# Kernel optimization log

Hardware: AMD Instinct MI355X
Metric: run time of the kernel (lower is better)

The kernel has to match this reference:

```python
import jax, jax.numpy as jnp
import numpy as np

B, T, N, M, D = 4, 2, 2048, 2048, 3

def _pairwise_sq(a, b):
    # a: [B,N,D], b: [B,M,D] -> squared euclidean distances [B,N,M]
    a2 = jnp.sum(a * a, axis=-1)
    b2 = jnp.sum(b * b, axis=-1)
    ab = jnp.einsum('bnd,bmd->bnm', a, b)
    return jnp.maximum(a2[:, :, None] + b2[:, None, :] - 2.0 * ab, 0.0)


def setup_inputs() -> dict:
    key = jax.random.key(0)
    k1, k2, k3, k4 = jax.random.split(key, 4)
    x = jax.random.uniform(k1, (B, T, N, D), dtype=jnp.float32)
    # m_hat is the frozen motion model's output; small motions keep chamfer mask active
    m_hat = jax.random.uniform(k2, (B, 1, N, D), dtype=jnp.float32) * 0.02
    y_hat0 = jax.random.uniform(k3, (B, 1, M, D), dtype=jnp.float32)
    y_hat1 = jax.random.uniform(k4, (B, 1, M, D), dtype=jnp.float32)
    return {'x': x, 'm_hat': m_hat, 'y_hat0': y_hat0, 'y_hat1': y_hat1}


def reference(x, m_hat, y_hat0, y_hat1):
    sg = jax.lax.stop_gradient
    x_t0 = x[:, 0, :, :3]              # [B,N,3]
    x_t1 = x[:, 1, :, :3]              # [B,N,3]
    x_t1_hat = x_t0 + m_hat[:, 0]      # [B,N,3]

    # chamfer(x_t1_hat, x_t1): squared NN distances both ways
    d = _pairwise_sq(x_t1_hat, x_t1)   # [B,N,N]
    dist1 = jnp.min(d, axis=-1)
    dist2 = jnp.min(d, axis=-2)
    loss_chamfer = dist1.mean(axis=-1) + dist2.mean(axis=-1)          # [B]
    mask_chamfer = sg((loss_chamfer < 0.1).astype(x.dtype))[:, None, None, None]

    y0 = y_hat0[:, 0]                  # [B,M,3]
    dists = jnp.sqrt(_pairwise_sq(y0, x_t0))                          # [B,M,N]
    x_cat = jnp.concatenate([x_t0, x_t1], axis=1)                     # [B,2N,3]
    dists2 = jnp.sqrt(_pairwise_sq(y0, x_cat))                        # [B,M,2N]

    min_dists = jnp.min(dists, axis=-1)        # [B,M]
    min_indices = jnp.argmin(dists, axis=-1)   # [B,M]
    min_dists2 = jnp.min(dists2, axis=-1)      # [B,M]

    mask_dist = sg((min_dists < 0.05).astype(x.dtype))[:, None, :, None]      # [B,1,M,1]
    mask_dist_neg = sg((min_dists2 > 0.2).astype(x.dtype))[:, None, :, None]  # [B,1,M,1]

    nearest_m = jnp.take_along_axis(m_hat[:, 0], min_indices[:, :, None], axis=1)  # [B,M,3]

    # chamfer(x_t0, y_hat0): only dist1 used, masked mean over entries < 0.1
    c1 = jnp.min(_pairwise_sq(x_t0, y0), axis=-1)                     # [B,N]
    sel = c1 < 0.1
    loss_dist = jnp.sum(jnp.where(sel, c1, 0.0)) / jnp.maximum(jnp.sum(sel.astype(c1.dtype)), 1.0)

    pred = (y_hat1 - y_hat0) * mask_chamfer * mask_dist               # [B,1,M,3]
    tgt = nearest_m[:, None, :, :] * mask_chamfer * mask_dist
    loss_dynamic = jnp.mean((pred - tgt) ** 2)

    my_hat_static = (y_hat1 - y_hat0) * mask_dist_neg
    loss_static = jnp.mean(my_hat_static ** 2)

    return (loss_dynamic, loss_static, loss_dist)
```

## Files before the change

kernel.cpp:

```cpp
#include <hip/hip_runtime.h>
#include <math.h>

#define BATCH 4
#define NPTS  2048
#define NT    256
#define ROWS_PT 4
#define CPB     64
#define COLCHUNKS (NPTS / CPB)
#define ROWHALVES 2
#define ROWS_TOT  (BATCH * NPTS)
#define RB_BLOCKS (ROWS_TOT / 128)

#define OFF_PD1   0
#define OFF_PD2   (COLCHUNKS * ROWS_TOT)
#define OFF_PC1   (2 * COLCHUNKS * ROWS_TOT)
#define OFF_PRM3  (3 * COLCHUNKS * ROWS_TOT)
#define OFF_PRM2  (4 * COLCHUNKS * ROWS_TOT)
#define OFF_BLK   (6 * COLCHUNKS * ROWS_TOT)
#define INF_BITS 0x7f800000u

typedef unsigned long long ull;

__device__ __forceinline__ float sqnorm3(float x, float y, float z) {
    return __fadd_rn(__fadd_rn(__fmul_rn(x, x), __fmul_rn(y, y)), __fmul_rn(z, z));
}

#define SRC_T0  0
#define SRC_T1  1
#define SRC_T1H 2
#define SRC_Y0  3

__device__ __forceinline__ float4 make_point(int src, bool col, int b, int i,
    const float* __restrict__ x, const float* __restrict__ m_hat,
    const float* __restrict__ y_hat0)
{
    float px, py, pz;
    if (src == SRC_Y0) {
        const float* p = y_hat0 + ((size_t)b * NPTS + i) * 3;
        px = p[0]; py = p[1]; pz = p[2];
    } else if (src == SRC_T1) {
        const float* p = x + ((size_t)(b * 2 + 1) * NPTS + i) * 3;
        px = p[0]; py = p[1]; pz = p[2];
    } else {
        const float* p = x + ((size_t)(b * 2 + 0) * NPTS + i) * 3;
        px = p[0]; py = p[1]; pz = p[2];
        if (src == SRC_T1H) {
            const float* mh = m_hat + ((size_t)b * NPTS + i) * 3;
            px += mh[0]; py += mh[1]; pz += mh[2];
        }
    }
    float w = sqnorm3(px, py, pz);
    if (col) { px *= -2.0f; py *= -2.0f; pz *= -2.0f; }
    return make_float4(px, py, pz, w);
}

__device__ __forceinline__ ull shfl_xor_u64(ull v, int m) {
    int lo = __shfl_xor((int)(v & 0xFFFFFFFFull), m);
    int hi = __shfl_xor((int)(v >> 32), m);
    return ((ull)(unsigned)hi << 32) | (unsigned)lo;
}

__device__ __forceinline__ float dist_sq_raw(const float4& a, const float4& q) {
    float s = a.x * q.x + a.y * q.y + a.z * q.z;
    float u = __fadd_rn(a.w, q.w);
    return __fadd_rn(u, s);
}

__global__ __launch_bounds__(NT) void pairwise_kernel(
    const float* __restrict__ x, const float* __restrict__ m_hat,
    const float* __restrict__ y_hat0, float* __restrict__ ws)
{
    __shared__ float4 tile[CPB];

    int tid = threadIdx.x;
    int rowHalf  = blockIdx.x >> 5;
    int colChunk = blockIdx.x & 31;
    int b    = blockIdx.y;
    int prob = blockIdx.z;

    int rsrc, csrc, outOff;
    switch (prob) {
        case 0:  rsrc = SRC_T1H; csrc = SRC_T1;  outOff = OFF_PD1;  break;
        case 1:  rsrc = SRC_T1;  csrc = SRC_T1H; outOff = OFF_PD2;  break;
        case 2:  rsrc = SRC_Y0;  csrc = SRC_T0;  outOff = -1;       break;
        case 3:  rsrc = SRC_Y0;  csrc = SRC_T1;  outOff = OFF_PRM3; break;
        default: rsrc = SRC_T0;  csrc = SRC_Y0;  outOff = OFF_PC1;  break;
    }

    int colBase = colChunk * CPB;
    if (tid < CPB) tile[tid] = make_point(csrc, true, b, colBase + tid, x, m_hat, y_hat0);

    int r0 = rowHalf * (NT * ROWS_PT) + tid;
    float4 a[ROWS_PT];
    #pragma unroll
    for (int k = 0; k < ROWS_PT; ++k)
        a[k] = make_point(rsrc, false, b, r0 + k * NT, x, m_hat, y_hat0);

    __syncthreads();

    if (prob == 2) {
        float best[ROWS_PT];
        int bestIdx[ROWS_PT];
        #pragma unroll
        for (int k = 0; k < ROWS_PT; ++k) { best[k] = __uint_as_float(INF_BITS); bestIdx[k] = 0; }
        for (int c = 0; c < CPB; ++c) {
            float4 q = tile[c];
            #pragma unroll
            for (int k = 0; k < ROWS_PT; ++k) {
                float d = fmaxf(dist_sq_raw(a[k], q), 0.0f);
                if (d < best[k]) { best[k] = d; bestIdx[k] = c; }
            }
        }
        ull* prm2 = (ull*)(ws + OFF_PRM2);
        #pragma unroll
        for (int k = 0; k < ROWS_PT; ++k) {
            ull key = ((ull)__float_as_uint(best[k]) << 32) |
                      (unsigned)(colBase + bestIdx[k]);
            prm2[(size_t)colChunk * ROWS_TOT + b * NPTS + r0 + k * NT] = key;
        }
    } else {
        float best[ROWS_PT];
        #pragma unroll
        for (int k = 0; k < ROWS_PT; ++k) best[k] = __uint_as_float(INF_BITS);
        for (int c = 0; c < CPB; ++c) {
            float4 q = tile[c];
            #pragma unroll
            for (int k = 0; k < ROWS_PT; ++k)
                best[k] = fminf(best[k], dist_sq_raw(a[k], q));
        }
        #pragma unroll
        for (int k = 0; k < ROWS_PT; ++k)
            ws[outOff + (size_t)colChunk * ROWS_TOT + b * NPTS + r0 + k * NT] = best[k];
    }
}

__global__ __launch_bounds__(NT) void rowreduce_kernel(
    const float* __restrict__ m_hat, const float* __restrict__ y_hat0,
    const float* __restrict__ y_hat1, float* __restrict__ ws)
{
    int tid  = threadIdx.x;
    int row  = blockIdx.x * 128 + (tid >> 1);
    int half = tid & 1;
    int b    = row >> 11;

    const ull* prm2 = (const ull*)(ws + OFF_PRM2);

    float d1m = __uint_as_float(INF_BITS), d2m = d1m, c1m = d1m, r3m = d1m;
    ull k2 = ~0ull;
    #pragma unroll
    for (int c = 0; c < 16; ++c) {
        int idx = (half * 16 + c) * ROWS_TOT + row;
        d1m = fminf(d1m, ws[OFF_PD1 + idx]);
        d2m = fminf(d2m, ws[OFF_PD2 + idx]);
        c1m = fminf(c1m, ws[OFF_PC1 + idx]);
        r3m = fminf(r3m, ws[OFF_PRM3 + idx]);
        ull kk = prm2[idx];
        k2 = (kk < k2) ? kk : k2;
    }
    d1m = fminf(d1m, __shfl_xor(d1m, 1));
    d2m = fminf(d2m, __shfl_xor(d2m, 1));
    c1m = fminf(c1m, __shfl_xor(c1m, 1));
    r3m = fminf(r3m, __shfl_xor(r3m, 1));
    { ull o = shfl_xor_u64(k2, 1); k2 = (o < k2) ? o : k2; }

    d1m = fmaxf(d1m, 0.0f);
    d2m = fmaxf(d2m, 0.0f);
    c1m = fmaxf(c1m, 0.0f);
    r3m = fmaxf(r3m, 0.0f);

    float d2sq = __uint_as_float((unsigned)(k2 >> 32));
    unsigned idxm = (unsigned)(k2 & 0xFFFFFFFFull);
    float md   = (sqrtf(d2sq) < 0.05f) ? 1.0f : 0.0f;
    float dcat = fminf(d2sq, r3m);
    float mneg = (sqrtf(dcat) > 0.2f) ? 1.0f : 0.0f;

    const float* p0 = y_hat0 + (size_t)row * 3;
    const float* p1 = y_hat1 + (size_t)row * 3;
    const float* nm = m_hat + ((size_t)b * NPTS + idxm) * 3;

    float dyn = 0.f, stat = 0.f;
    #pragma unroll
    for (int k = 0; k < 3; ++k) {
        float diff = p1[k] - p0[k];
        float e = md * (diff - nm[k]);
        dyn += e * e;
        float s = mneg * diff;
        stat += s * s;
    }
    float cs = (c1m < 0.1f) ? c1m : 0.f;
    float cn = (c1m < 0.1f) ? 1.f  : 0.f;
    float s1 = d1m, s2 = d2m;
    if (half) { s1 = s2 = cs = cn = dyn = stat = 0.f; }

    #pragma unroll
    for (int off = 32; off > 0; off >>= 1) {
        s1  += __shfl_down(s1,  off);
        s2  += __shfl_down(s2,  off);
        cs  += __shfl_down(cs,  off);
        cn  += __shfl_down(cn,  off);
        dyn += __shfl_down(dyn, off);
        stat+= __shfl_down(stat,off);
    }
    __shared__ float sm[4][6];
    int wv = tid >> 6, ln = tid & 63;
    if (ln == 0) {
        sm[wv][0] = s1; sm[wv][1] = s2; sm[wv][2] = cs;
        sm[wv][3] = cn; sm[wv][4] = dyn; sm[wv][5] = stat;
    }
    __syncthreads();
    if (tid == 0) {
        #pragma unroll
        for (int j = 0; j < 6; ++j)
            ws[OFF_BLK + blockIdx.x * 8 + j] = sm[0][j] + sm[1][j] + sm[2][j] + sm[3][j];
    }
}

__global__ void final_kernel(const float* __restrict__ ws, float* __restrict__ out)
{
    int lane = threadIdx.x;
    float v[6];
    #pragma unroll
    for (int j = 0; j < 6; ++j) v[j] = ws[OFF_BLK + lane * 8 + j];
    #pragma unroll
    for (int off = 8; off > 0; off >>= 1) {
        #pragma unroll
        for (int j = 0; j < 6; ++j) {
            float t = __shfl_down(v[j], off);
            if (((lane & 15) + off) < 16) v[j] += t;
        }
    }
    __shared__ float bs[4][6];
    if ((lane & 15) == 0) {
        #pragma unroll
        for (int j = 0; j < 6; ++j) bs[lane >> 4][j] = v[j];
    }
    __syncthreads();
    if (lane == 0) {
        float dyn = 0.f, stat = 0.f, cs = 0.f, cn = 0.f;
        for (int b = 0; b < 4; ++b) {
            float lc = bs[b][0] / (float)NPTS + bs[b][1] / (float)NPTS;
            float maskc = (lc < 0.1f) ? 1.0f : 0.0f;
            dyn  += maskc * bs[b][4];
            stat += bs[b][5];
            cs   += bs[b][2];
            cn   += bs[b][3];
        }
        const float denom = (float)(BATCH * NPTS * 3);
        out[0] = dyn / denom;
        out[1] = stat / denom;
        out[2] = cs / fmaxf(cn, 1.0f);
    }
}

extern "C" void kernel_launch(void* const* d_in, const int* in_sizes, int n_in,
                              void* d_out, int out_size, void* d_ws, size_t ws_size,
                              hipStream_t stream)
{
    const float* x      = (const float*)d_in[0];
    const float* m_hat  = (const float*)d_in[1];
    const float* y_hat0 = (const float*)d_in[2];
    const float* y_hat1 = (const float*)d_in[3];
    float* ws  = (float*)d_ws;
    float* out = (float*)d_out;

    pairwise_kernel<<<dim3(ROWHALVES * COLCHUNKS, BATCH, 5), dim3(NT), 0, stream>>>(
        x, m_hat, y_hat0, ws);
    rowreduce_kernel<<<dim3(RB_BLOCKS), dim3(NT), 0, stream>>>(
        m_hat, y_hat0, y_hat1, ws);
    final_kernel<<<dim3(1), dim3(64), 0, stream>>>(ws, out);
}
```

Baseline: 84.67 us.

## Share distance tiles for row and column mins, register-tile 8x8, fuse final reduce

Each distance matrix is now computed once, and both its row minima and column minima are reduced from the same 128x128 tile. This cuts the pairwise work from five matrix passes to three. Each thread now computes an 8x8 register tile from padded shared-memory row and column tiles, using shuffle and shared reductions for the partial minima. The separate final kernel is removed: the last rowreduce block, found through an atomic counter, does the global reduction. In exchange, the new counter needs a reset inside the pairwise kernel and some column partials are computed in swapped operand order, so rounding may differ slightly.

```diff
diff --git a/kernel.cpp b/kernel.cpp
--- a/kernel.cpp
+++ b/kernel.cpp
@@ -4,20 +4,23 @@
 #define BATCH 4
 #define NPTS  2048
 #define NT    256
-#define ROWS_PT 4
-#define CPB     64
-#define COLCHUNKS (NPTS / CPB)
-#define ROWHALVES 2
-#define ROWS_TOT  (BATCH * NPTS)
+#define TM    128
+#define TN    128
+#define CH    (NPTS / TN)
+#define ROWS_TOT (BATCH * NPTS)
 #define RB_BLOCKS (ROWS_TOT / 128)
-
-#define OFF_PD1   0
-#define OFF_PD2   (COLCHUNKS * ROWS_TOT)
-#define OFF_PC1   (2 * COLCHUNKS * ROWS_TOT)
-#define OFF_PRM3  (3 * COLCHUNKS * ROWS_TOT)
-#define OFF_PRM2  (4 * COLCHUNKS * ROWS_TOT)
-#define OFF_BLK   (6 * COLCHUNKS * ROWS_TOT)
+#define CHUNK_F (CH * ROWS_TOT)
+
+#define OFF_AROW 0
+#define OFF_ACOL (1 * CHUNK_F)
+#define OFF_BCOL (2 * CHUNK_F)
+#define OFF_CROW (3 * CHUNK_F)
+#define OFF_BKEY (4 * CHUNK_F)
+#define OFF_BLK  (6 * CHUNK_F)
+#define OFF_CTR  (OFF_BLK + RB_BLOCKS * 8)
 #define INF_BITS 0x7f800000u
+
+#define PIDX(i) ((i) + ((i) >> 3))
 
 typedef unsigned long long ull;
 
@@ -70,91 +73,187 @@
     const float* __restrict__ x, const float* __restrict__ m_hat,
     const float* __restrict__ y_hat0, float* __restrict__ ws)
 {
-    __shared__ float4 tile[CPB];
+    __shared__ float4 rowT[TM + TM / 8];
+    __shared__ float4 colT[TN + TN / 8];
+    __shared__ float  colRed[4][TN];
 
     int tid = threadIdx.x;
-    int rowHalf  = blockIdx.x >> 5;
-    int colChunk = blockIdx.x & 31;
-    int b    = blockIdx.y;
-    int prob = blockIdx.z;
-
-    int rsrc, csrc, outOff;
-    switch (prob) {
-        case 0:  rsrc = SRC_T1H; csrc = SRC_T1;  outOff = OFF_PD1;  break;
-        case 1:  rsrc = SRC_T1;  csrc = SRC_T1H; outOff = OFF_PD2;  break;
-        case 2:  rsrc = SRC_Y0;  csrc = SRC_T0;  outOff = -1;       break;
-        case 3:  rsrc = SRC_Y0;  csrc = SRC_T1;  outOff = OFF_PRM3; break;
-        default: rsrc = SRC_T0;  csrc = SRC_Y0;  outOff = OFF_PC1;  break;
-    }
-
-    int colBase = colChunk * CPB;
-    if (tid < CPB) tile[tid] = make_point(csrc, true, b, colBase + tid, x, m_hat, y_hat0);
-
-    int r0 = rowHalf * (NT * ROWS_PT) + tid;
-    float4 a[ROWS_PT];
-    #pragma unroll
-    for (int k = 0; k < ROWS_PT; ++k)
-        a[k] = make_point(rsrc, false, b, r0 + k * NT, x, m_hat, y_hat0);
-
+    int rowChunk = blockIdx.x >> 4;
+    int colChunk = blockIdx.x & 15;
+    int b   = blockIdx.y;
+    int mat = blockIdx.z;
+
+    if (blockIdx.x == 0 && b == 0 && mat == 0 && tid == 0)
+        ((unsigned*)ws)[OFF_CTR] = 0u;
+
+    int rsrc, csrc;
+    if (mat == 0)      { rsrc = SRC_T1H; csrc = SRC_T1; }
+    else if (mat == 1) { rsrc = SRC_Y0;  csrc = SRC_T0; }
+    else               { rsrc = SRC_Y0;  csrc = SRC_T1; }
+
+    int rowBase = rowChunk * TM;
+    int colBase = colChunk * TN;
+
+    if (tid < TM) {
+        rowT[PIDX(tid)] = make_point(rsrc, false, b, rowBase + tid, x, m_hat, y_hat0);
+    } else {
+        int t = tid - TM;
+        colT[PIDX(t)] = make_point(csrc, true, b, colBase + t, x, m_hat, y_hat0);
+    }
     __syncthreads();
 
-    if (prob == 2) {
-        float best[ROWS_PT];
-        int bestIdx[ROWS_PT];
-        #pragma unroll
-        for (int k = 0; k < ROWS_PT; ++k) { best[k] = __uint_as_float(INF_BITS); bestIdx[k] = 0; }
-        for (int c = 0; c < CPB; ++c) {
-            float4 q = tile[c];
-            #pragma unroll
-            for (int k = 0; k < ROWS_PT; ++k) {
-                float d = fmaxf(dist_sq_raw(a[k], q), 0.0f);
-                if (d < best[k]) { best[k] = d; bestIdx[k] = c; }
-            }
-        }
-        ull* prm2 = (ull*)(ws + OFF_PRM2);
-        #pragma unroll
-        for (int k = 0; k < ROWS_PT; ++k) {
-            ull key = ((ull)__float_as_uint(best[k]) << 32) |
-                      (unsigned)(colBase + bestIdx[k]);
-            prm2[(size_t)colChunk * ROWS_TOT + b * NPTS + r0 + k * NT] = key;
+    int tx = tid & 15, ty = tid >> 4;
+    float4 a[8], q[8];
+    #pragma unroll
+    for (int i = 0; i < 8; ++i) a[i] = rowT[PIDX(ty * 8 + i)];
+    #pragma unroll
+    for (int j = 0; j < 8; ++j) q[j] = colT[PIDX(tx * 8 + j)];
+
+    if (mat == 1) {
+        float rbest[8], cmin[8];
+        int ridx[8];
+        #pragma unroll
+        for (int i = 0; i < 8; ++i) {
+            rbest[i] = __uint_as_float(INF_BITS);
+            cmin[i]  = __uint_as_float(INF_BITS);
+            ridx[i]  = 0;
+        }
+        #pragma unroll
+        for (int j = 0; j < 8; ++j) {
+            #pragma unroll
+            for (int i = 0; i < 8; ++i) {
+                float d = dist_sq_raw(a[i], q[j]);
+                cmin[j] = fminf(cmin[j], d);
+                float dc = fmaxf(d, 0.0f);
+                if (dc < rbest[i]) { rbest[i] = dc; ridx[i] = j; }
+            }
+        }
+        ull key[8];
+        #pragma unroll
+        for (int i = 0; i < 8; ++i)
+            key[i] = ((ull)__float_as_uint(rbest[i]) << 32) |
+                     (unsigned)(colBase + tx * 8 + ridx[i]);
+        #pragma unroll
+        for (int m = 1; m < 16; m <<= 1) {
+            #pragma unroll
+            for (int i = 0; i < 8; ++i) {
+                ull o = shfl_xor_u64(key[i], m);
+                key[i] = (o < key[i]) ? o : key[i];
+            }
+        }
+        if (tx == 0) {
+            ull* o = (ull*)(ws + OFF_BKEY) +
+                     (size_t)colChunk * ROWS_TOT + b * NPTS + rowBase + ty * 8;
+            #pragma unroll
+            for (int i = 0; i < 8; ++i) o[i] = key[i];
+        }
+        #pragma unroll
+        for (int j = 0; j < 8; ++j) {
+            cmin[j] = fminf(cmin[j], __shfl_xor(cmin[j], 16));
+            cmin[j] = fminf(cmin[j], __shfl_xor(cmin[j], 32));
+        }
+        int w = tid >> 6;
+        if ((tid & 63) < 16) {
+            #pragma unroll
+            for (int j = 0; j < 8; ++j) colRed[w][tx * 8 + j] = cmin[j];
+        }
+        __syncthreads();
+        if (tid < TN) {
+            float v = fminf(fminf(colRed[0][tid], colRed[1][tid]),
+                            fminf(colRed[2][tid], colRed[3][tid]));
+            ws[OFF_BCOL + (size_t)rowChunk * ROWS_TOT + b * NPTS + colBase + tid] = v;
+        }
+    } else if (mat == 0) {
+        float rmin[8], cmin[8];
+        #pragma unroll
+        for (int i = 0; i < 8; ++i) {
+            rmin[i] = __uint_as_float(INF_BITS);
+            cmin[i] = __uint_as_float(INF_BITS);
+        }
+        #pragma unroll
+        for (int j = 0; j < 8; ++j) {
+            #pragma unroll
+            for (int i = 0; i < 8; ++i) {
+                float d = dist_sq_raw(a[i], q[j]);
+                rmin[i] = fminf(rmin[i], d);
+                cmin[j] = fminf(cmin[j], d);
+            }
+        }
+        #pragma unroll
+        for (int m = 1; m < 16; m <<= 1) {
+            #pragma unroll
+            for (int i = 0; i < 8; ++i)
+                rmin[i] = fminf(rmin[i], __shfl_xor(rmin[i], m));
+        }
+        if (tx == 0) {
+            float* o = ws + OFF_AROW +
+                       (size_t)colChunk * ROWS_TOT + b * NPTS + rowBase + ty * 8;
+            *(float4*)(o)     = make_float4(rmin[0], rmin[1], rmin[2], rmin[3]);
+            *(float4*)(o + 4) = make_float4(rmin[4], rmin[5], rmin[6], rmin[7]);
+        }
+        #pragma unroll
+        for (int j = 0; j < 8; ++j) {
+            cmin[j] = fminf(cmin[j], __shfl_xor(cmin[j], 16));
+            cmin[j] = fminf(cmin[j], __shfl_xor(cmin[j], 32));
+        }
+        int w = tid >> 6;
+        if ((tid & 63) < 16) {
+            #pragma unroll
+            for (int j = 0; j < 8; ++j) colRed[w][tx * 8 + j] = cmin[j];
+        }
+        __syncthreads();
+        if (tid < TN) {
+            float v = fminf(fminf(colRed[0][tid], colRed[1][tid]),
+                            fminf(colRed[2][tid], colRed[3][tid]));
+            ws[OFF_ACOL + (size_t)rowChunk * ROWS_TOT + b * NPTS + colBase + tid] = v;
         }
     } else {
-        float best[ROWS_PT];
-        #pragma unroll
-        for (int k = 0; k < ROWS_PT; ++k) best[k] = __uint_as_float(INF_BITS);
-        for (int c = 0; c < CPB; ++c) {
-            float4 q = tile[c];
-            #pragma unroll
-            for (int k = 0; k < ROWS_PT; ++k)
-                best[k] = fminf(best[k], dist_sq_raw(a[k], q));
-        }
-        #pragma unroll
-        for (int k = 0; k < ROWS_PT; ++k)
-            ws[outOff + (size_t)colChunk * ROWS_TOT + b * NPTS + r0 + k * NT] = best[k];
+        float rmin[8];
+        #pragma unroll
+        for (int i = 0; i < 8; ++i) rmin[i] = __uint_as_float(INF_BITS);
+        #pragma unroll
+        for (int j = 0; j < 8; ++j) {
+            #pragma unroll
+            for (int i = 0; i < 8; ++i)
+                rmin[i] = fminf(rmin[i], dist_sq_raw(a[i], q[j]));
+        }
+        #pragma unroll
+        for (int m = 1; m < 16; m <<= 1) {
+            #pragma unroll
+            for (int i = 0; i < 8; ++i)
+                rmin[i] = fminf(rmin[i], __shfl_xor(rmin[i], m));
+        }
+        if (tx == 0) {
+            float* o = ws + OFF_CROW +
+                       (size_t)colChunk * ROWS_TOT + b * NPTS + rowBase + ty * 8;
+            *(float4*)(o)     = make_float4(rmin[0], rmin[1], rmin[2], rmin[3]);
+            *(float4*)(o + 4) = make_float4(rmin[4], rmin[5], rmin[6], rmin[7]);
+        }
     }
 }
 
 __global__ __launch_bounds__(NT) void rowreduce_kernel(
     const float* __restrict__ m_hat, const float* __restrict__ y_hat0,
-    const float* __restrict__ y_hat1, float* __restrict__ ws)
+    const float* __restrict__ y_hat1, float* __restrict__ ws,
+    float* __restrict__ out)
 {
     int tid  = threadIdx.x;
     int row  = blockIdx.x * 128 + (tid >> 1);
     int half = tid & 1;
     int b    = row >> 11;
 
-    const ull* prm2 = (const ull*)(ws + OFF_PRM2);
+    const ull* bkey = (const ull*)(ws + OFF_BKEY);
 
     float d1m = __uint_as_float(INF_BITS), d2m = d1m, c1m = d1m, r3m = d1m;
     ull k2 = ~0ull;
     #pragma unroll
-    for (int c = 0; c < 16; ++c) {
-        int idx = (half * 16 + c) * ROWS_TOT + row;
-        d1m = fminf(d1m, ws[OFF_PD1 + idx]);
-        d2m = fminf(d2m, ws[OFF_PD2 + idx]);
-        c1m = fminf(c1m, ws[OFF_PC1 + idx]);
-        r3m = fminf(r3m, ws[OFF_PRM3 + idx]);
-        ull kk = prm2[idx];
+    for (int c = 0; c < 8; ++c) {
+        int idx = (half * 8 + c) * ROWS_TOT + row;
+        d1m = fminf(d1m, ws[OFF_AROW + idx]);
+        d2m = fminf(d2m, ws[OFF_ACOL + idx]);
+        c1m = fminf(c1m, ws[OFF_BCOL + idx]);
+        r3m = fminf(r3m, ws[OFF_CROW + idx]);
+        ull kk = bkey[idx];
         k2 = (kk < k2) ? kk : k2;
     }
     d1m = fminf(d1m, __shfl_xor(d1m, 1));
@@ -202,6 +301,7 @@
         stat+= __shfl_down(stat,off);
     }
     __shared__ float sm[4][6];
+    __shared__ int lastBlock;
     int wv = tid >> 6, ln = tid & 63;
     if (ln == 0) {
         sm[wv][0] = s1; sm[wv][1] = s2; sm[wv][2] = cs;
@@ -210,45 +310,62 @@
     __syncthreads();
     if (tid == 0) {
         #pragma unroll
+        for (int j = 0; j < 6; ++j) {
+            float v = sm[0][j] + sm[1][j] + sm[2][j] + sm[3][j];
+            __hip_atomic_store(ws + OFF_BLK + blockIdx.x * 8 + j, v,
+                               __ATOMIC_RELAXED, __HIP_MEMORY_SCOPE_AGENT);
+        }
+        __threadfence();
+        unsigned old = atomicAdd(((unsigned*)ws) + OFF_CTR, 1u);
+        lastBlock = (old == RB_BLOCKS - 1) ? 1 : 0;
+    }
+    __syncthreads();
+
+    if (lastBlock != 0 && tid < 64) {
+        __threadfence();
+        int lane = tid;
+        float v[6];
+        #pragma unroll
         for (int j = 0; j < 6; ++j)
-            ws[OFF_BLK + blockIdx.x * 8 + j] = sm[0][j] + sm[1][j] + sm[2][j] + sm[3][j];
-    }
-}
-
-__global__ void final_kernel(const float* __restrict__ ws, float* __restrict__ out)
-{
-    int lane = threadIdx.x;
-    float v[6];
-    #pragma unroll
-    for (int j = 0; j < 6; ++j) v[j] = ws[OFF_BLK + lane * 8 + j];
-    #pragma unroll
-    for (int off = 8; off > 0; off >>= 1) {
+            v[j] = __hip_atomic_load(ws + OFF_BLK + lane * 8 + j,
+                                     __ATOMIC_RELAXED, __HIP_MEMORY_SCOPE_AGENT);
+        #pragma unroll
+        for (int off = 8; off > 0; off >>= 1) {
+            #pragma unroll
+            for (int j = 0; j < 6; ++j) {
+                float t = __shfl_down(v[j], off);
+                if (((lane & 15) + off) < 16) v[j] += t;
+            }
+        }
+        float g1[6], g2[6], g3[6];
         #pragma unroll
         for (int j = 0; j < 6; ++j) {
-            float t = __shfl_down(v[j], off);
-            if (((lane & 15) + off) < 16) v[j] += t;
-        }
-    }
-    __shared__ float bs[4][6];
-    if ((lane & 15) == 0) {
-        #pragma unroll
-        for (int j = 0; j < 6; ++j) bs[lane >> 4][j] = v[j];
-    }
-    __syncthreads();
-    if (lane == 0) {
-        float dyn = 0.f, stat = 0.f, cs = 0.f, cn = 0.f;
-        for (int b = 0; b < 4; ++b) {
-            float lc = bs[b][0] / (float)NPTS + bs[b][1] / (float)NPTS;
-            float maskc = (lc < 0.1f) ? 1.0f : 0.0f;
-            dyn  += maskc * bs[b][4];
-            stat += bs[b][5];
-            cs   += bs[b][2];
-            cn   += bs[b][3];
-        }
-        const float denom = (float)(BATCH * NPTS * 3);
-        out[0] = dyn / denom;
-        out[1] = stat / denom;
-        out[2] = cs / fmaxf(cn, 1.0f);
+            g1[j] = __shfl(v[j], 16);
+            g2[j] = __shfl(v[j], 32);
+            g3[j] = __shfl(v[j], 48);
+        }
+        if (lane == 0) {
+            float bsm[4][6];
+            #pragma unroll
+            for (int j = 0; j < 6; ++j) {
+                bsm[0][j] = v[j];  bsm[1][j] = g1[j];
+                bsm[2][j] = g2[j]; bsm[3][j] = g3[j];
+            }
+            float dyn2 = 0.f, stat2 = 0.f, cs2 = 0.f, cn2 = 0.f;
+            #pragma unroll
+            for (int bb = 0; bb < 4; ++bb) {
+                float lc = bsm[bb][0] / (float)NPTS + bsm[bb][1] / (float)NPTS;
+                float maskc = (lc < 0.1f) ? 1.0f : 0.0f;
+                dyn2  += maskc * bsm[bb][4];
+                stat2 += bsm[bb][5];
+                cs2   += bsm[bb][2];
+                cn2   += bsm[bb][3];
+            }
+            const float denom = (float)(BATCH * NPTS * 3);
+            out[0] = dyn2 / denom;
+            out[1] = stat2 / denom;
+            out[2] = cs2 / fmaxf(cn2, 1.0f);
+        }
     }
 }
 
@@ -263,9 +380,8 @@
     float* ws  = (float*)d_ws;
     float* out = (float*)d_out;
 
-    pairwise_kernel<<<dim3(ROWHALVES * COLCHUNKS, BATCH, 5), dim3(NT), 0, stream>>>(
+    pairwise_kernel<<<dim3(CH * CH, BATCH, 3), dim3(NT), 0, stream>>>(
         x, m_hat, y_hat0, ws);
     rowreduce_kernel<<<dim3(RB_BLOCKS), dim3(NT), 0, stream>>>(
-        m_hat, y_hat0, y_hat1, ws);
-    final_kernel<<<dim3(1), dim3(64), 0, stream>>>(ws, out);
-}
+        m_hat, y_hat0, y_hat1, ws, out);
+}
```

Measured after the change: 86.07 us. About the same (+1.7%).
